# Optimization experiments

Measured on AMD Instinct MI355X. Metric: run time of the kernel, lower is better.

The kernel has to match this reference:

```python
import jax, jax.numpy as jnp
import numpy as np

D_MODEL = 256
N_HEADS = 8
D_FFN = 1024
B, N = 4, 1024
HEAD_DIM = D_MODEL // N_HEADS
LN_EPS = 1e-5


def _ln(x, g, b):
    mu = jnp.mean(x, axis=-1, keepdims=True)
    var = jnp.var(x, axis=-1, keepdims=True)
    return (x - mu) * jax.lax.rsqrt(var + LN_EPS) * g + b


def setup_inputs() -> dict:
    key = jax.random.key(0)
    ks = jax.random.split(key, 16)
    s = 0.02
    return {
        "embed": jax.random.normal(ks[0], (B, N, D_MODEL), jnp.float32),
        "refer_bbox": jax.random.uniform(ks[1], (B, N, 4), jnp.float32),
        "dist": jax.random.uniform(ks[2], (B, N, N), jnp.float32),
        "query_pos": jax.random.normal(ks[3], (B, N, D_MODEL), jnp.float32),
        "in_proj_w": jax.random.normal(ks[4], (3 * D_MODEL, D_MODEL), jnp.float32) * s,
        "in_proj_b": jnp.zeros((3 * D_MODEL,), jnp.float32),
        "out_w": jax.random.normal(ks[5], (D_MODEL, D_MODEL), jnp.float32) * s,
        "out_b": jnp.zeros((D_MODEL,), jnp.float32),
        "tau_w": jax.random.normal(ks[6], (N_HEADS, D_MODEL), jnp.float32) * s,
        "tau_b": jax.random.uniform(ks[7], (N_HEADS,), jnp.float32, 0.0, 2.0),
        "w1": jax.random.normal(ks[8], (D_FFN, D_MODEL), jnp.float32) * s,
        "b1": jnp.zeros((D_FFN,), jnp.float32),
        "w2": jax.random.normal(ks[9], (D_MODEL, D_FFN), jnp.float32) * s,
        "b2": jnp.zeros((D_MODEL,), jnp.float32),
        "g1": jnp.ones((D_MODEL,), jnp.float32),
        "beta1": jnp.zeros((D_MODEL,), jnp.float32),
        "g2": jnp.ones((D_MODEL,), jnp.float32),
        "beta2": jnp.zeros((D_MODEL,), jnp.float32),
    }


def reference(embed, refer_bbox, dist, query_pos, in_proj_w, in_proj_b, out_w, out_b,
              tau_w, tau_b, w1, b1, w2, b2, g1, beta1, g2, beta2):
    # tau: (B, N, H) -> (B, H, N); additive bias mask[b,h,i,j] = dist[b,i,j] * tau[b,h,i]
    tau = (embed @ tau_w.T + tau_b).transpose(0, 2, 1)
    bias = dist[:, None, :, :] * tau[..., None]  # (B, H, N, N)

    qk = embed + query_pos  # q = k = embed + pos, v = embed
    wq, wk, wv = jnp.split(in_proj_w, 3, axis=0)
    bq, bk, bv = jnp.split(in_proj_b, 3, axis=0)
    q = (qk @ wq.T + bq).reshape(B, N, N_HEADS, HEAD_DIM)
    k = (qk @ wk.T + bk).reshape(B, N, N_HEADS, HEAD_DIM)
    v = (embed @ wv.T + bv).reshape(B, N, N_HEADS, HEAD_DIM)

    scores = jnp.einsum("bihd,bjhd->bhij", q, k) / np.sqrt(HEAD_DIM) + bias
    attn = jax.nn.softmax(scores, axis=-1)
    ctx = jnp.einsum("bhij,bjhd->bihd", attn, v).reshape(B, N, D_MODEL)
    tgt = ctx @ out_w.T + out_b

    x = _ln(embed + tgt, g1, beta1)
    ffn = jax.nn.relu(x @ w1.T + b1) @ w2.T + b2
    return _ln(x + ffn, g2, beta2)
```

## Files before the change

kernel.cpp:

```cpp
#include <hip/hip_runtime.h>
#include <math.h>

#define D_MODEL 256
#define N_HEADS 8
#define HEAD_DIM 32
#define D_FFN   1024
#define BB      4
#define NN      1024
#define M_TOT   (BB * NN)
#define LN_EPS  1e-5f

#define QSCALE_LOG2E 0.2550348612f
#define LOG2E        1.4426950408889634f

typedef float f32x4 __attribute__((ext_vector_type(4)));
typedef short bf16x8 __attribute__((ext_vector_type(8)));

__device__ __forceinline__ unsigned short f2bf(float f) {
    unsigned int u = __float_as_uint(f);
    unsigned int r = (u + 0x7fffu + ((u >> 16) & 1u)) >> 16;
    return (unsigned short)r;
}
__device__ __forceinline__ ushort4 pack4(float4 v) {
    ushort4 o; o.x = f2bf(v.x); o.y = f2bf(v.y); o.z = f2bf(v.z); o.w = f2bf(v.w);
    return o;
}
__device__ __forceinline__ float fast_exp2(float x) {
#if __has_builtin(__builtin_amdgcn_exp2f)
    return __builtin_amdgcn_exp2f(x);
#else
    return exp2f(x);
#endif
}
__device__ __forceinline__ float bf2f(unsigned short s) {
    return __uint_as_float(((unsigned int)s) << 16);
}

__global__ __launch_bounds__(256)
void prep_all_kernel(const float4* __restrict__ e, const float4* __restrict__ qp,
                     ushort4* __restrict__ ebf, ushort4* __restrict__ qkbf,
                     const float4* __restrict__ inw4, ushort4* __restrict__ o_inw,
                     const float* __restrict__ outw, const float* __restrict__ w1,
                     const float* __restrict__ w2,
                     unsigned short* __restrict__ o_outwf,
                     unsigned short* __restrict__ o_w1f,
                     unsigned short* __restrict__ o_w2f,
                     const float4* __restrict__ tauw, ushort4* __restrict__ o_taupad) {
    if (blockIdx.x < 1024) {
        int i = blockIdx.x * 256 + threadIdx.x;
        float4 ev = e[i], pv = qp[i];
        ebf[i] = pack4(ev);
        float4 s = make_float4(ev.x + pv.x, ev.y + pv.y, ev.z + pv.z, ev.w + pv.w);
        qkbf[i] = pack4(s);
    } else if (blockIdx.x < 1216) {
        int i = (blockIdx.x - 1024) * 256 + threadIdx.x;
        o_inw[i] = pack4(inw4[i]);
    } else if (blockIdx.x < 1504) {
        int fid = (blockIdx.x - 1216) * 256 + threadIdx.x;
        const float* W; unsigned short* dst; int K;
        if (fid < 8192)       { W = outw; dst = o_outwf; K = 256; }
        else if (fid < 40960) { W = w1;   dst = o_w1f;   K = 256;  fid -= 8192; }
        else                  { W = w2;   dst = o_w2f;   K = 1024; fid -= 40960; }
        const int lane = fid & 63;
        const int t = fid >> 6;
        const int kk = t % (K / 32);
        const int n16 = t / (K / 32);
        const int row = n16 * 16 + (lane & 15);
        const int col = kk * 32 + (lane >> 4) * 8;
        const float* src = &W[(size_t)row * K + col];
        float4 s0 = *(const float4*)src, s1 = *(const float4*)(src + 4);
        *(ushort4*)&dst[(size_t)fid * 8]     = pack4(s0);
        *(ushort4*)&dst[(size_t)fid * 8 + 4] = pack4(s1);
    } else {
        int q = (blockIdx.x - 1504) * 256 + threadIdx.x;
        if (q < 512) o_taupad[q] = pack4(tauw[q]);
        else { ushort4 z = {0, 0, 0, 0}; o_taupad[q] = z; }
    }
}

__global__ __launch_bounds__(256)
void qkv_mfma_kernel(const unsigned short* __restrict__ qk_bf,
                     const unsigned short* __restrict__ emb_bf,
                     const unsigned short* __restrict__ inw_bf,
                     const unsigned short* __restrict__ taupad,
                     const float* __restrict__ in_proj_b, const float* __restrict__ tau_b,
                     unsigned short* __restrict__ qb, unsigned short* __restrict__ kb,
                     unsigned short* __restrict__ vbT, float* __restrict__ taub) {
    const int w    = threadIdx.x >> 6;
    const int lane = threadIdx.x & 63;
    const int l16 = lane & 15, l4 = lane >> 4;
    const int n0 = blockIdx.x * 64;
    const int m0 = blockIdx.y * 64;
    const int wm = (w >> 1) * 32, wn = (w & 1) * 32;

    const unsigned short* A = (blockIdx.x < 8) ? qk_bf : emb_bf;
    const unsigned short* W0 = (n0 < 768) ? &inw_bf[(size_t)(n0 + wn + l16) * D_MODEL]
                                          : &taupad[(size_t)(wn + l16) * D_MODEL];
    const unsigned short* Ar0 = &A[(size_t)(m0 + wm + l16) * D_MODEL];

    f32x4 acc[2][2] = {};
    #pragma unroll
    for (int k0 = 0; k0 < D_MODEL; k0 += 32) {
        bf16x8 a0 = *(const bf16x8*)&Ar0[k0 + l4 * 8];
        bf16x8 a1 = *(const bf16x8*)&Ar0[16 * D_MODEL + k0 + l4 * 8];
        bf16x8 b0 = *(const bf16x8*)&W0[k0 + l4 * 8];
        bf16x8 b1 = *(const bf16x8*)&W0[16 * D_MODEL + k0 + l4 * 8];
        acc[0][0] = __builtin_amdgcn_mfma_f32_16x16x32_bf16(a0, b0, acc[0][0], 0, 0, 0);
        acc[0][1] = __builtin_amdgcn_mfma_f32_16x16x32_bf16(a0, b1, acc[0][1], 0, 0, 0);
        acc[1][0] = __builtin_amdgcn_mfma_f32_16x16x32_bf16(a1, b0, acc[1][0], 0, 0, 0);
        acc[1][1] = __builtin_amdgcn_mfma_f32_16x16x32_bf16(a1, b1, acc[1][1], 0, 0, 0);
    }

    #pragma unroll
    for (int i = 0; i < 2; i++) {
        #pragma unroll
        for (int j = 0; j < 2; j++) {
            #pragma unroll
            for (int r = 0; r < 4; r++) {
                const int m = m0 + wm + i * 16 + l4 * 4 + r;
                const int b = m >> 10, nrow = m & 1023;
                const int c = n0 + wn + j * 16 + l16;
                float v = acc[i][j][r];
                if (c < 256) {
                    v = (v + in_proj_b[c]) * QSCALE_LOG2E;
                    int h = c >> 5, d = c & 31;
                    qb[((size_t)(b * N_HEADS + h) * NN + nrow) * HEAD_DIM + d] = f2bf(v);
                } else if (c < 512) {
                    v += in_proj_b[c];
                    int cc = c - 256; int h = cc >> 5, d = cc & 31;
                    kb[((size_t)(b * N_HEADS + h) * NN + nrow) * HEAD_DIM + d] = f2bf(v);
                } else if (c < 768) {
                    v += in_proj_b[c];
                    int cc = c - 512; int h = cc >> 5, d = cc & 31;
                    vbT[((size_t)(b * N_HEADS + h) * HEAD_DIM + d) * NN + nrow] = f2bf(v);
                } else if (c < 776) {
                    v = (v + tau_b[c - 768]) * LOG2E;
                    taub[(size_t)(b * N_HEADS + (c - 768)) * NN + nrow] = v;
                }
            }
        }
    }
}

__global__ __launch_bounds__(256)
void attn_mfma_kernel(const unsigned short* __restrict__ qb,
                      const unsigned short* __restrict__ kb,
                      const unsigned short* __restrict__ vbT,
                      const float* __restrict__ taub,
                      const float* __restrict__ dist,
                      unsigned short* __restrict__ Opart,
                      float* __restrict__ lpart) {
    __shared__ unsigned short Kf[4][4][512];
    __shared__ unsigned short Vf[4][2][2][512];
    __shared__ unsigned short Plds[4][16 * 72];
    const int w    = threadIdx.x >> 6;
    const int lane = threadIdx.x & 63;
    const int l16  = lane & 15;
    const int l4   = lane >> 4;
    const int bh = blockIdx.y;
    const int b = bh >> 3;
    const int z = blockIdx.z;
    const int i0 = blockIdx.x * 64 + w * 16;
    const int jbase = z * 256;

    {
        const int kt = w;
        const unsigned short* kb_z = &kb[((size_t)bh * NN + jbase + kt * 64) * HEAD_DIM];
        #pragma unroll
        for (int s = 0; s < 4; s++) {
            bf16x8 kv = *(const bf16x8*)&kb_z[(size_t)(l16 * 4 + s) * HEAD_DIM + l4 * 8];
            *(bf16x8*)&Kf[kt][s][lane * 8] = kv;
        }
        const unsigned short* vb_z = &vbT[(size_t)bh * HEAD_DIM * NN + jbase + kt * 64];
        #pragma unroll
        for (int c = 0; c < 2; c++)
            #pragma unroll
            for (int h2 = 0; h2 < 2; h2++) {
                bf16x8 vv = *(const bf16x8*)&vb_z[(size_t)(h2 * 16 + l16) * NN + c * 32 + l4 * 8];
                *(bf16x8*)&Vf[kt][c][h2][lane * 8] = vv;
            }
    }

    const f32x4 zero = {0.f, 0.f, 0.f, 0.f};
    bf16x8 qf = *(const bf16x8*)&qb[((size_t)bh * NN + i0 + l16) * HEAD_DIM + l4 * 8];
    float tau_r[4];
    const float* drow[4];
    #pragma unroll
    for (int r = 0; r < 4; r++) {
        tau_r[r] = taub[(size_t)bh * NN + i0 + l4 * 4 + r];
        drow[r] = &dist[((size_t)b * NN + i0 + l4 * 4 + r) * NN + jbase];
    }
    float l_acc[4] = {0.f, 0.f, 0.f, 0.f};
    f32x4 O0 = zero, O1 = zero;
    unsigned short* pw = &Plds[w][0];

    __syncthreads();

    for (int kt = 0; kt < 4; kt++) {
        const int j0 = kt * 64;
        f32x4 dd4[4];
        #pragma unroll
        for (int r = 0; r < 4; r++)
            dd4[r] = *(const f32x4*)&drow[r][j0 + l16 * 4];

        float parr[4][4];
        #pragma unroll
        for (int s = 0; s < 4; s++) {
            bf16x8 kfr = *(const bf16x8*)&Kf[kt][s][lane * 8];
            f32x4 S = __builtin_amdgcn_mfma_f32_16x16x32_bf16(qf, kfr, zero, 0, 0, 0);
            #pragma unroll
            for (int r = 0; r < 4; r++) {
                const float p = fast_exp2(S[r] + dd4[r][s] * tau_r[r]);
                parr[s][r] = p;
                l_acc[r] += p;
            }
        }

        #pragma unroll
        for (int r = 0; r < 4; r++) {
            ushort4 pk;
            pk.x = f2bf(parr[0][r]); pk.y = f2bf(parr[1][r]);
            pk.z = f2bf(parr[2][r]); pk.w = f2bf(parr[3][r]);
            *(ushort4*)&pw[(l4 * 4 + r) * 72 + l16 * 4] = pk;
        }
        asm volatile("s_waitcnt lgkmcnt(0)" ::: "memory");
        #pragma unroll
        for (int c = 0; c < 2; c++) {
            bf16x8 pf = *(const bf16x8*)&pw[l16 * 72 + c * 32 + l4 * 8];
            bf16x8 v0 = *(const bf16x8*)&Vf[kt][c][0][lane * 8];
            bf16x8 v1 = *(const bf16x8*)&Vf[kt][c][1][lane * 8];
            O0 = __builtin_amdgcn_mfma_f32_16x16x32_bf16(pf, v0, O0, 0, 0, 0);
            O1 = __builtin_amdgcn_mfma_f32_16x16x32_bf16(pf, v1, O1, 0, 0, 0);
        }
    }

    #pragma unroll
    for (int msk = 1; msk < 16; msk <<= 1)
        #pragma unroll
        for (int r = 0; r < 4; r++)
            l_acc[r] += __shfl_xor(l_acc[r], msk, 16);

    #pragma unroll
    for (int r = 0; r < 4; r++) {
        const int i = i0 + l4 * 4 + r;
        unsigned short* crow = &Opart[((size_t)(z * 32 + bh) * NN + i) * 32];
        crow[l16]      = f2bf(O0[r]);
        crow[16 + l16] = f2bf(O1[r]);
        if (l16 == 0)
            lpart[(size_t)(z * 32 + bh) * NN + i] = l_acc[r];
    }
}

__global__ __launch_bounds__(1024)
void post_kernel(const unsigned short* __restrict__ Opart, const float* __restrict__ lpart,
                 const unsigned short* __restrict__ outwf,
                 const float* __restrict__ out_b, const float* __restrict__ embed,
                 const float* __restrict__ g1, const float* __restrict__ beta1,
                 const unsigned short* __restrict__ w1f, const float* __restrict__ b1,
                 const unsigned short* __restrict__ w2f, const float* __restrict__ b2,
                 const float* __restrict__ g2, const float* __restrict__ beta2,
                 float* __restrict__ out) {
    __shared__ float Lh[16][8];
    __shared__ unsigned short cs[16][264];
    __shared__ unsigned short xs[16][264];
    __shared__ unsigned short fs[16][1032];
    __shared__ float sums[16][4][4][2];

    const int tid = threadIdx.x;
    const int w = tid >> 6, lane = tid & 63;
    const int l16 = lane & 15, l4 = lane >> 4;
    const int m0 = blockIdx.x * 16;
    const int b = m0 >> 10;

    if (tid < 128) {
        const int row = tid >> 3, h = tid & 7;
        const int i = (m0 + row) & 1023;
        const int rowA = ((b * 8 + h) << 10) + i;
        float l = 0.f;
        #pragma unroll
        for (int z = 0; z < 4; z++) l += lpart[z * 32768 + rowA];
        Lh[row][h] = 1.0f / l;
    }
    __syncthreads();

    if (tid < 512) {
        const int row = tid >> 5;
        const int d0 = (tid & 31) * 8;
        const int h = d0 >> 5;
        const int dd = d0 & 31;
        const int i = (m0 + row) & 1023;
        const int rowA = ((b * 8 + h) << 10) + i;
        float s[8] = {};
        #pragma unroll
        for (int z = 0; z < 4; z++) {
            bf16x8 u = *(const bf16x8*)&Opart[((size_t)(z * 32768 + rowA)) * 32 + dd];
            #pragma unroll
            for (int j = 0; j < 8; j++) s[j] += bf2f((unsigned short)u[j]);
        }
        const float li = Lh[row][h];
        #pragma unroll
        for (int j = 0; j < 8; j++)
            cs[row][d0 + j] = f2bf(s[j] * li);
    }
    __syncthreads();

    const int cA = w * 16 + l16;
    f32x4 a0 = {}, a1 = {};
    {
        const unsigned short* ofr = &outwf[(size_t)w * 8 * 512 + lane * 8];
        #pragma unroll
        for (int kk = 0; kk < 4; kk++) {
            const int k0 = kk * 32, k1 = 128 + kk * 32;
            bf16x8 x0 = *(const bf16x8*)&cs[l16][k0 + l4 * 8];
            bf16x8 b0 = *(const bf16x8*)&ofr[kk * 512];
            bf16x8 x1 = *(const bf16x8*)&cs[l16][k1 + l4 * 8];
            bf16x8 b1v = *(const bf16x8*)&ofr[(4 + kk) * 512];
            a0 = __builtin_amdgcn_mfma_f32_16x16x32_bf16(x0, b0, a0, 0, 0, 0);
            a1 = __builtin_amdgcn_mfma_f32_16x16x32_bf16(x1, b1v, a1, 0, 0, 0);
        }
    }
    float xv[4];
    {
        float s_r[4] = {0.f, 0.f, 0.f, 0.f}, q_r[4] = {0.f, 0.f, 0.f, 0.f};
        const float bs = out_b[cA];
        #pragma unroll
        for (int r = 0; r < 4; r++) {
            const int m = m0 + l4 * 4 + r;
            const float t = a0[r] + a1[r] + bs + embed[(size_t)m * D_MODEL + cA];
            xv[r] = t; s_r[r] += t; q_r[r] += t * t;
        }
        #pragma unroll
        for (int msk = 1; msk < 16; msk <<= 1)
            #pragma unroll
            for (int r = 0; r < 4; r++) {
                s_r[r] += __shfl_xor(s_r[r], msk, 16);
                q_r[r] += __shfl_xor(q_r[r], msk, 16);
            }
        if (l16 == 0)
            #pragma unroll
            for (int r = 0; r < 4; r++) {
                sums[w][l4][r][0] = s_r[r];
                sums[w][l4][r][1] = q_r[r];
            }
    }
    __syncthreads();
    #pragma unroll
    for (int r = 0; r < 4; r++) {
        float s = 0.f, q = 0.f;
        #pragma unroll
        for (int ww = 0; ww < 16; ww++) { s += sums[ww][l4][r][0]; q += sums[ww][l4][r][1]; }
        const float mu = s * (1.0f / D_MODEL);
        const float var = q * (1.0f / D_MODEL) - mu * mu;
        const float rstd = rsqrtf(var + LN_EPS);
        const float ov = (xv[r] - mu) * rstd * g1[cA] + beta1[cA];
        xv[r] = ov;
        xs[l4 * 4 + r][cA] = f2bf(ov);
    }
    __syncthreads();

    f32x4 accB[4] = {};
    {
        const unsigned short* wfr = &w1f[(size_t)(w * 4) * 8 * 512 + lane * 8];
        bf16x8 wf[4], wfn[4];
        #pragma unroll
        for (int j = 0; j < 4; j++)
            wf[j] = *(const bf16x8*)&wfr[(size_t)j * 8 * 512];
        #pragma unroll
        for (int kk = 0; kk < 8; kk++) {
            if (kk < 7) {
                #pragma unroll
                for (int j = 0; j < 4; j++)
                    wfn[j] = *(const bf16x8*)&wfr[((size_t)j * 8 + kk + 1) * 512];
            }
            bf16x8 a = *(const bf16x8*)&xs[l16][kk * 32 + l4 * 8];
            #pragma unroll
            for (int j = 0; j < 4; j++)
                accB[j] = __builtin_amdgcn_mfma_f32_16x16x32_bf16(a, wf[j], accB[j], 0, 0, 0);
            if (kk < 7) {
                #pragma unroll
                for (int j = 0; j < 4; j++) wf[j] = wfn[j];
            }
        }
    }
    #pragma unroll
    for (int j = 0; j < 4; j++) {
        const int fc = w * 64 + j * 16 + l16;
        const float bs = b1[fc];
        #pragma unroll
        for (int r = 0; r < 4; r++)
            fs[l4 * 4 + r][fc] = f2bf(fmaxf(accB[j][r] + bs, 0.f));
    }
    __syncthreads();

    f32x4 c0 = {}, c1 = {};
    {
        const unsigned short* wfr = &w2f[(size_t)w * 32 * 512 + lane * 8];
        bf16x8 wb0 = *(const bf16x8*)&wfr[0];
        bf16x8 wb1 = *(const bf16x8*)&wfr[16 * 512];
        #pragma unroll
        for (int kk = 0; kk < 16; kk++) {
            const int k0 = kk * 32, k1 = 512 + kk * 32;
            bf16x8 cur0 = wb0, cur1 = wb1;
            if (kk < 15) {
                wb0 = *(const bf16x8*)&wfr[(size_t)(kk + 1) * 512];
                wb1 = *(const bf16x8*)&wfr[(size_t)(16 + kk + 1) * 512];
            }
            bf16x8 f0 = *(const bf16x8*)&fs[l16][k0 + l4 * 8];
            bf16x8 f1 = *(const bf16x8*)&fs[l16][k1 + l4 * 8];
            c0 = __builtin_amdgcn_mfma_f32_16x16x32_bf16(f0, cur0, c0, 0, 0, 0);
            c1 = __builtin_amdgcn_mfma_f32_16x16x32_bf16(f1, cur1, c1, 0, 0, 0);
        }
    }
    float v2[4];
    {
        float s_r[4] = {0.f, 0.f, 0.f, 0.f}, q_r[4] = {0.f, 0.f, 0.f, 0.f};
        const float bs = b2[cA];
        #pragma unroll
        for (int r = 0; r < 4; r++) {
            const float t = c0[r] + c1[r] + bs + xv[r];
            v2[r] = t; s_r[r] += t; q_r[r] += t * t;
        }
        #pragma unroll
        for (int msk = 1; msk < 16; msk <<= 1)
            #pragma unroll
            for (int r = 0; r < 4; r++) {
                s_r[r] += __shfl_xor(s_r[r], msk, 16);
                q_r[r] += __shfl_xor(q_r[r], msk, 16);
            }
        if (l16 == 0)
            #pragma unroll
            for (int r = 0; r < 4; r++) {
                sums[w][l4][r][0] = s_r[r];
                sums[w][l4][r][1] = q_r[r];
            }
    }
    __syncthreads();
    #pragma unroll
    for (int r = 0; r < 4; r++) {
        float s = 0.f, q = 0.f;
        #pragma unroll
        for (int ww = 0; ww < 16; ww++) { s += sums[ww][l4][r][0]; q += sums[ww][l4][r][1]; }
        const float mu = s * (1.0f / D_MODEL);
        const float var = q * (1.0f / D_MODEL) - mu * mu;
        const float rstd = rsqrtf(var + LN_EPS);
        const int m = m0 + l4 * 4 + r;
        out[(size_t)m * D_MODEL + cA] = (v2[r] - mu) * rstd * g2[cA] + beta2[cA];
    }
}

extern "C" void kernel_launch(void* const* d_in, const int* in_sizes, int n_in,
                              void* d_out, int out_size, void* d_ws, size_t ws_size,
                              hipStream_t stream) {
    const float* embed     = (const float*)d_in[0];
    const float* dist      = (const float*)d_in[2];
    const float* query_pos = (const float*)d_in[3];
    const float* in_proj_w = (const float*)d_in[4];
    const float* in_proj_b = (const float*)d_in[5];
    const float* out_w     = (const float*)d_in[6];
    const float* out_b     = (const float*)d_in[7];
    const float* tau_w     = (const float*)d_in[8];
    const float* tau_b     = (const float*)d_in[9];
    const float* w1        = (const float*)d_in[10];
    const float* b1        = (const float*)d_in[11];
    const float* w2        = (const float*)d_in[12];
    const float* b2        = (const float*)d_in[13];
    const float* g1        = (const float*)d_in[14];
    const float* beta1     = (const float*)d_in[15];
    const float* g2        = (const float*)d_in[16];
    const float* beta2     = (const float*)d_in[17];
    float* out = (float*)d_out;

    char* ws = (char*)d_ws;
    const size_t MB = 1024 * 1024;
    const size_t KB = 1024;
    unsigned short* emb_bf  = (unsigned short*)(ws);
    unsigned short* qk_bf   = (unsigned short*)(ws + 2 * MB);
    unsigned short* qb      = (unsigned short*)(ws + 4 * MB);
    unsigned short* kb      = (unsigned short*)(ws + 6 * MB);
    unsigned short* vbT     = (unsigned short*)(ws + 8 * MB);
    float*          taub    = (float*)(ws + 10 * MB);
    unsigned short* inw_bf  = (unsigned short*)(ws + 11 * MB);
    unsigned short* outwf   = (unsigned short*)(ws + 11 * MB + 512 * KB);
    unsigned short* w1f     = (unsigned short*)(ws + 12 * MB);
    unsigned short* w2f     = (unsigned short*)(ws + 12 * MB + 512 * KB);
    unsigned short* taupad  = (unsigned short*)(ws + 13 * MB);
    unsigned short* Opart   = (unsigned short*)(ws + 14 * MB);
    float*          lpart   = (float*)(ws + 22 * MB);

    prep_all_kernel<<<dim3(1520), dim3(256), 0, stream>>>(
        (const float4*)embed, (const float4*)query_pos,
        (ushort4*)emb_bf, (ushort4*)qk_bf,
        (const float4*)in_proj_w, (ushort4*)inw_bf,
        out_w, w1, w2, outwf, w1f, w2f,
        (const float4*)tau_w, (ushort4*)taupad);

    qkv_mfma_kernel<<<dim3(13, M_TOT / 64), dim3(256), 0, stream>>>(
        qk_bf, emb_bf, inw_bf, taupad, in_proj_b, tau_b, qb, kb, vbT, taub);

    attn_mfma_kernel<<<dim3(NN / 64, BB * N_HEADS, 4), dim3(256), 0, stream>>>(
        qb, kb, vbT, taub, dist, Opart, lpart);

    post_kernel<<<dim3(M_TOT / 16), dim3(1024), 0, stream>>>(
        Opart, lpart, outwf, out_b, embed, g1, beta1,
        w1f, b1, w2f, b2, g2, beta2, out);
}
```

Before: 164.2 us.

## Halve attention key-split to two partitions and vectorize LayerNorm partial-sum reads

The attention kernel now splits the key dimension into 2 chunks of 512 instead of 4 chunks of 256. Each block processes two 256-key halves, reloading K/V into shared memory between them behind extra barriers. This halves the partial output and row-sum traffic that post_kernel must read and reduce, at the cost of half as many attention blocks and two more syncs per block. Separately, the LayerNorm partial sums in shared memory are transposed so each row's 16 warp partials sit contiguously and can be read with vector loads.

```diff
diff --git a/kernel.cpp b/kernel.cpp
--- a/kernel.cpp
+++ b/kernel.cpp
@@ -161,23 +161,22 @@
     const int b = bh >> 3;
     const int z = blockIdx.z;
     const int i0 = blockIdx.x * 64 + w * 16;
-    const int jbase = z * 256;
+    const int jbase = z * 512;
 
     {
-        const int kt = w;
-        const unsigned short* kb_z = &kb[((size_t)bh * NN + jbase + kt * 64) * HEAD_DIM];
+        const unsigned short* kb_z = &kb[((size_t)bh * NN + jbase + w * 64) * HEAD_DIM];
         #pragma unroll
         for (int s = 0; s < 4; s++) {
             bf16x8 kv = *(const bf16x8*)&kb_z[(size_t)(l16 * 4 + s) * HEAD_DIM + l4 * 8];
-            *(bf16x8*)&Kf[kt][s][lane * 8] = kv;
-        }
-        const unsigned short* vb_z = &vbT[(size_t)bh * HEAD_DIM * NN + jbase + kt * 64];
+            *(bf16x8*)&Kf[w][s][lane * 8] = kv;
+        }
+        const unsigned short* vb_z = &vbT[(size_t)bh * HEAD_DIM * NN + jbase + w * 64];
         #pragma unroll
         for (int c = 0; c < 2; c++)
             #pragma unroll
             for (int h2 = 0; h2 < 2; h2++) {
                 bf16x8 vv = *(const bf16x8*)&vb_z[(size_t)(h2 * 16 + l16) * NN + c * 32 + l4 * 8];
-                *(bf16x8*)&Vf[kt][c][h2][lane * 8] = vv;
+                *(bf16x8*)&Vf[w][c][h2][lane * 8] = vv;
             }
     }
 
@@ -196,41 +195,63 @@
 
     __syncthreads();
 
-    for (int kt = 0; kt < 4; kt++) {
-        const int j0 = kt * 64;
-        f32x4 dd4[4];
-        #pragma unroll
-        for (int r = 0; r < 4; r++)
-            dd4[r] = *(const f32x4*)&drow[r][j0 + l16 * 4];
-
-        float parr[4][4];
-        #pragma unroll
-        for (int s = 0; s < 4; s++) {
-            bf16x8 kfr = *(const bf16x8*)&Kf[kt][s][lane * 8];
-            f32x4 S = __builtin_amdgcn_mfma_f32_16x16x32_bf16(qf, kfr, zero, 0, 0, 0);
+    for (int half = 0; half < 2; half++) {
+        const int hb = half * 256;
+        if (half) {
+            __syncthreads();
+            const unsigned short* kb_z = &kb[((size_t)bh * NN + jbase + 256 + w * 64) * HEAD_DIM];
+            #pragma unroll
+            for (int s = 0; s < 4; s++) {
+                bf16x8 kv = *(const bf16x8*)&kb_z[(size_t)(l16 * 4 + s) * HEAD_DIM + l4 * 8];
+                *(bf16x8*)&Kf[w][s][lane * 8] = kv;
+            }
+            const unsigned short* vb_z = &vbT[(size_t)bh * HEAD_DIM * NN + jbase + 256 + w * 64];
+            #pragma unroll
+            for (int c = 0; c < 2; c++)
+                #pragma unroll
+                for (int h2 = 0; h2 < 2; h2++) {
+                    bf16x8 vv = *(const bf16x8*)&vb_z[(size_t)(h2 * 16 + l16) * NN + c * 32 + l4 * 8];
+                    *(bf16x8*)&Vf[w][c][h2][lane * 8] = vv;
+                }
+            __syncthreads();
+        }
+
+        for (int kt = 0; kt < 4; kt++) {
+            const int j0 = hb + kt * 64;
+            f32x4 dd4[4];
+            #pragma unroll
+            for (int r = 0; r < 4; r++)
+                dd4[r] = *(const f32x4*)&drow[r][j0 + l16 * 4];
+
+            float parr[4][4];
+            #pragma unroll
+            for (int s = 0; s < 4; s++) {
+                bf16x8 kfr = *(const bf16x8*)&Kf[kt][s][lane * 8];
+                f32x4 S = __builtin_amdgcn_mfma_f32_16x16x32_bf16(qf, kfr, zero, 0, 0, 0);
+                #pragma unroll
+                for (int r = 0; r < 4; r++) {
+                    const float p = fast_exp2(S[r] + dd4[r][s] * tau_r[r]);
+                    parr[s][r] = p;
+                    l_acc[r] += p;
+                }
+            }
+
             #pragma unroll
             for (int r = 0; r < 4; r++) {
-                const float p = fast_exp2(S[r] + dd4[r][s] * tau_r[r]);
-                parr[s][r] = p;
-                l_acc[r] += p;
-            }
-        }
-
-        #pragma unroll
-        for (int r = 0; r < 4; r++) {
-            ushort4 pk;
-            pk.x = f2bf(parr[0][r]); pk.y = f2bf(parr[1][r]);
-            pk.z = f2bf(parr[2][r]); pk.w = f2bf(parr[3][r]);
-            *(ushort4*)&pw[(l4 * 4 + r) * 72 + l16 * 4] = pk;
-        }
-        asm volatile("s_waitcnt lgkmcnt(0)" ::: "memory");
-        #pragma unroll
-        for (int c = 0; c < 2; c++) {
-            bf16x8 pf = *(const bf16x8*)&pw[l16 * 72 + c * 32 + l4 * 8];
-            bf16x8 v0 = *(const bf16x8*)&Vf[kt][c][0][lane * 8];
-            bf16x8 v1 = *(const bf16x8*)&Vf[kt][c][1][lane * 8];
-            O0 = __builtin_amdgcn_mfma_f32_16x16x32_bf16(pf, v0, O0, 0, 0, 0);
-            O1 = __builtin_amdgcn_mfma_f32_16x16x32_bf16(pf, v1, O1, 0, 0, 0);
+                ushort4 pk;
+                pk.x = f2bf(parr[0][r]); pk.y = f2bf(parr[1][r]);
+                pk.z = f2bf(parr[2][r]); pk.w = f2bf(parr[3][r]);
+                *(ushort4*)&pw[(l4 * 4 + r) * 72 + l16 * 4] = pk;
+            }
+            asm volatile("s_waitcnt lgkmcnt(0)" ::: "memory");
+            #pragma unroll
+            for (int c = 0; c < 2; c++) {
+                bf16x8 pf = *(const bf16x8*)&pw[l16 * 72 + c * 32 + l4 * 8];
+                bf16x8 v0 = *(const bf16x8*)&Vf[kt][c][0][lane * 8];
+                bf16x8 v1 = *(const bf16x8*)&Vf[kt][c][1][lane * 8];
+                O0 = __builtin_amdgcn_mfma_f32_16x16x32_bf16(pf, v0, O0, 0, 0, 0);
+                O1 = __builtin_amdgcn_mfma_f32_16x16x32_bf16(pf, v1, O1, 0, 0, 0);
+            }
         }
     }
 
@@ -264,7 +285,7 @@
     __shared__ unsigned short cs[16][264];
     __shared__ unsigned short xs[16][264];
     __shared__ unsigned short fs[16][1032];
-    __shared__ float sums[16][4][4][2];
+    __shared__ float sums[4][4][16][2];
 
     const int tid = threadIdx.x;
     const int w = tid >> 6, lane = tid & 63;
@@ -276,10 +297,7 @@
         const int row = tid >> 3, h = tid & 7;
         const int i = (m0 + row) & 1023;
         const int rowA = ((b * 8 + h) << 10) + i;
-        float l = 0.f;
-        #pragma unroll
-        for (int z = 0; z < 4; z++) l += lpart[z * 32768 + rowA];
-        Lh[row][h] = 1.0f / l;
+        Lh[row][h] = 1.0f / (lpart[rowA] + lpart[32768 + rowA]);
     }
     __syncthreads();
 
@@ -292,7 +310,7 @@
         const int rowA = ((b * 8 + h) << 10) + i;
         float s[8] = {};
         #pragma unroll
-        for (int z = 0; z < 4; z++) {
+        for (int z = 0; z < 2; z++) {
             bf16x8 u = *(const bf16x8*)&Opart[((size_t)(z * 32768 + rowA)) * 32 + dd];
             #pragma unroll
             for (int j = 0; j < 8; j++) s[j] += bf2f((unsigned short)u[j]);
@@ -339,16 +357,20 @@
         if (l16 == 0)
             #pragma unroll
             for (int r = 0; r < 4; r++) {
-                sums[w][l4][r][0] = s_r[r];
-                sums[w][l4][r][1] = q_r[r];
+                sums[l4][r][w][0] = s_r[r];
+                sums[l4][r][w][1] = q_r[r];
             }
     }
     __syncthreads();
     #pragma unroll
     for (int r = 0; r < 4; r++) {
+        const float* sp = &sums[l4][r][0][0];
         float s = 0.f, q = 0.f;
         #pragma unroll
-        for (int ww = 0; ww < 16; ww++) { s += sums[ww][l4][r][0]; q += sums[ww][l4][r][1]; }
+        for (int ww = 0; ww < 8; ww++) {
+            f32x4 v = *(const f32x4*)&sp[ww * 4];
+            s += v[0] + v[2]; q += v[1] + v[3];
+        }
         const float mu = s * (1.0f / D_MODEL);
         const float var = q * (1.0f / D_MODEL) - mu * mu;
         const float rstd = rsqrtf(var + LN_EPS);
@@ -430,16 +452,20 @@
         if (l16 == 0)
             #pragma unroll
             for (int r = 0; r < 4; r++) {
-                sums[w][l4][r][0] = s_r[r];
-                sums[w][l4][r][1] = q_r[r];
+                sums[l4][r][w][0] = s_r[r];
+                sums[l4][r][w][1] = q_r[r];
             }
     }
     __syncthreads();
     #pragma unroll
     for (int r = 0; r < 4; r++) {
+        const float* sp = &sums[l4][r][0][0];
         float s = 0.f, q = 0.f;
         #pragma unroll
-        for (int ww = 0; ww < 16; ww++) { s += sums[ww][l4][r][0]; q += sums[ww][l4][r][1]; }
+        for (int ww = 0; ww < 8; ww++) {
+            f32x4 v = *(const f32x4*)&sp[ww * 4];
+            s += v[0] + v[2]; q += v[1] + v[3];
+        }
         const float mu = s * (1.0f / D_MODEL);
         const float var = q * (1.0f / D_MODEL) - mu * mu;
         const float rstd = rsqrtf(var + LN_EPS);
@@ -497,7 +523,7 @@
     qkv_mfma_kernel<<<dim3(13, M_TOT / 64), dim3(256), 0, stream>>>(
         qk_bf, emb_bf, inw_bf, taupad, in_proj_b, tau_b, qb, kb, vbT, taub);
 
-    attn_mfma_kernel<<<dim3(NN / 64, BB * N_HEADS, 4), dim3(256), 0, stream>>>(
+    attn_mfma_kernel<<<dim3(NN / 64, BB * N_HEADS, 2), dim3(256), 0, stream>>>(
         qb, kb, vbT, taub, dist, Opart, lpart);
 
     post_kernel<<<dim3(M_TOT / 16), dim3(1024), 0, stream>>>(
```

After: 169.4 us. 3.1% more time.
